# Performance work log

Measured on AMD Instinct MI355X. Metric: run time of the kernel, lower is better.

## Reference

```python
import jax, jax.numpy as jnp
import numpy as np

NUM_HEADS = 8
SIGMA = 1.0
LAMBDA_INIT = 0.1
GAMMA_INIT = 0.001


def _pos_encoding(H, W, d_model):
    # 2D sinusoidal encoding: first half encodes x (width), second half y (height)
    d = d_model // 2
    div = jnp.exp(jnp.arange(0, d, 2, dtype=jnp.float32) * (-np.log(10000.0) / d))
    xs = jnp.arange(W, dtype=jnp.float32)[:, None] * div  # (W, d//2)
    ys = jnp.arange(H, dtype=jnp.float32)[:, None] * div  # (H, d//2)
    pe_x = jnp.stack([jnp.sin(xs), jnp.cos(xs)], axis=-1).reshape(W, d)
    pe_y = jnp.stack([jnp.sin(ys), jnp.cos(ys)], axis=-1).reshape(H, d)
    pe = jnp.concatenate([
        jnp.broadcast_to(pe_x[None, :, :], (H, W, d)),
        jnp.broadcast_to(pe_y[:, None, :], (H, W, d)),
    ], axis=-1)
    return pe  # (H, W, d_model)


def _distance_map(H, W, sigma):
    # exp(-euclidean_dist / sigma) between all flattened pixel positions
    yy, xx = jnp.meshgrid(jnp.arange(H, dtype=jnp.float32), jnp.arange(W, dtype=jnp.float32), indexing='ij')
    coords = jnp.stack([yy.reshape(-1), xx.reshape(-1)], axis=-1)  # (HW, 2)
    d2 = jnp.sum((coords[:, None, :] - coords[None, :, :]) ** 2, axis=-1)
    return jnp.exp(-jnp.sqrt(d2) / sigma)  # (HW, HW)


def _conv1x1(x, w, b):
    # 1x1 conv == channel matmul; x: (B,C,H,W), w: (O,C), b: (O,)
    return jnp.einsum('bchw,oc->bohw', x, w) + b[None, :, None, None]


def setup_inputs() -> dict:
    key = jax.random.key(0)
    ks = jax.random.split(key, 9)
    B, C, H, W = 2, 256, 48, 48
    d_model = 256
    inp = {
        'x': jax.random.normal(ks[0], (B, C, H, W), dtype=jnp.float32),
        'Wq': jax.random.normal(ks[1], (d_model, C), dtype=jnp.float32) * 0.01,
        'bq': jnp.zeros((d_model,), dtype=jnp.float32),
        'Wk': jax.random.normal(ks[2], (d_model, C), dtype=jnp.float32) * 0.01,
        'bk': jnp.zeros((d_model,), dtype=jnp.float32),
        'Wv': jax.random.normal(ks[3], (d_model, C), dtype=jnp.float32) * 0.01,
        'bv': jnp.zeros((d_model,), dtype=jnp.float32),
        'Wo': jax.random.normal(ks[4], (C, d_model), dtype=jnp.float32) * 0.01,
        'bo': jnp.zeros((C,), dtype=jnp.float32),
        'lambda_dist': jnp.float32(LAMBDA_INIT),
        'gamma': jnp.float32(GAMMA_INIT),
    }
    return inp


def reference(x, Wq, bq, Wk, bk, Wv, bv, Wo, bo, lambda_dist, gamma):
    B, C, H, W = x.shape
    d_model = Wq.shape[0]
    d_k = d_model // NUM_HEADS
    pe = _pos_encoding(H, W, d_model).transpose(2, 0, 1)[None]  # (1, d_model, H, W)
    dm = _distance_map(H, W, SIGMA)                              # (HW, HW)

    q = _conv1x1(x, Wq, bq) + pe
    k = _conv1x1(x, Wk, bk) + pe
    v = _conv1x1(x, Wv, bv)

    def heads(t):
        return t.reshape(B, NUM_HEADS, d_k, H * W).transpose(0, 1, 3, 2)  # (B,h,HW,d_k)

    Q, K, V = heads(q), heads(k), heads(v)
    scores = jnp.einsum('bhnd,bhmd->bhnm', Q, K) / jnp.sqrt(jnp.float32(d_k))
    scores = scores + (lambda_dist * dm)[None, None]  # 'exp' distance prior bias
    attn = jax.nn.softmax(scores, axis=-1)
    out = jnp.einsum('bhnm,bhmd->bhnd', attn, V)
    out = out.transpose(0, 1, 3, 2).reshape(B, d_model, H, W)
    fused = gamma * out  # simple weighted fusion, single (self) branch
    return x + _conv1x1(fused, Wo, bo)
```

## Files before the change

### kernel.cpp

```cpp
#include <hip/hip_runtime.h>

#define HW 2304
#define SW 48
#define DMODEL 256
#define NHEADS 8
#define DK 32
#define BATCH 2

typedef unsigned short u16;
typedef __attribute__((ext_vector_type(8))) short short8;
typedef __attribute__((ext_vector_type(4))) float f32x4;

__device__ __forceinline__ float bf2f(u16 v) {
  union { unsigned int u; float f; } c; c.u = ((unsigned int)v) << 16; return c.f;
}
__device__ __forceinline__ float lo2f(unsigned int u) {
  union { unsigned int u; float f; } c; c.u = u << 16; return c.f;
}
__device__ __forceinline__ float hi2f(unsigned int u) {
  union { unsigned int u; float f; } c; c.u = u & 0xffff0000u; return c.f;
}
__device__ __forceinline__ u16 f2bf(float f) {
  union { unsigned int u; float f; } c; c.f = f;
  unsigned int u = c.u;
  unsigned int r = (u + 0x7FFFu + ((u >> 16) & 1u)) >> 16;
  return (u16)r;
}
__device__ __forceinline__ unsigned int pkbf(float a, float b) {
  union { float f; unsigned int u; } ca, cb;
  ca.f = a; cb.f = b;
  return __builtin_amdgcn_perm(ca.u, cb.u, 0x03020706u);
}
__device__ __forceinline__ float ex2(float x) {
#if __has_builtin(__builtin_amdgcn_exp2f)
  return __builtin_amdgcn_exp2f(x);
#else
  return __expf(x * 0.6931471805599453f);
#endif
}
__device__ __forceinline__ int div48(int n) { return (n * 87382) >> 22; }
__device__ __forceinline__ int div3(int n) { return (n * 171) >> 9; }
__device__ __forceinline__ int swz(int row, int k) {
  return ((row >> 4) << 12) + ((k >> 3) << 7) + ((row & 15) << 3) + (k & 7);
}

#define LOG2E 1.4426950408889634f

__global__ __launch_bounds__(256) void prep_kernel(
    const float* __restrict__ x,
    const float* __restrict__ Wq, const float* __restrict__ Wk,
    const float* __restrict__ Wv, const float* __restrict__ Wo,
    const float* __restrict__ lam_p,
    u16* __restrict__ xt, u16* __restrict__ Wb, u16* __restrict__ et) {
  int bid = blockIdx.x;
  int t = threadIdx.x;
  if (bid < 288) {
    int b = bid / 144, r = bid % 144;
    int c0 = (r / 36) * 64, n0 = (r % 36) * 64;
    __shared__ u16 sh[64][72];
#pragma unroll
    for (int p = 0; p < 4; ++p) {
      int row = (t >> 4) + p * 16;
      int col4 = (t & 15) * 4;
      float4 v = *(const float4*)(x + (size_t)(b * DMODEL + c0 + row) * HW +
                                  n0 + col4);
      sh[col4 + 0][row] = f2bf(v.x);
      sh[col4 + 1][row] = f2bf(v.y);
      sh[col4 + 2][row] = f2bf(v.z);
      sh[col4 + 3][row] = f2bf(v.w);
    }
    __syncthreads();
    u16* xtb = xt + (size_t)b * HW * DMODEL;
#pragma unroll
    for (int q = 0; q < 2; ++q) {
      int nrow = t >> 2;
      int c8 = (t & 3) * 8 + q * 32;
      *(uint4*)(xtb + swz(n0 + nrow, c0 + c8)) = *(const uint4*)&sh[nrow][c8];
    }
  } else if (bid < 544) {
    int idx = (bid - 288) * 1024 + t * 4;
    int which = idx >> 16, off = idx & 65535;
    int m = off >> 8, k = off & 255;
    const float* src = (which == 0) ? Wq : (which == 1) ? Wk
                       : (which == 2) ? Wv : Wo;
    float4 v = *(const float4*)(src + off);
    ushort4 ov;
    ov.x = f2bf(v.x); ov.y = f2bf(v.y); ov.z = f2bf(v.z); ov.w = f2bf(v.w);
    *(ushort4*)(Wb + which * 65536 + swz(m, k)) = ov;
  } else {
    int id = (bid - 544) * 256 + t;
    if (id < 15200) {
      int flat = id * 8;
      int tile = flat >> 8;
      int within = flat & 255;
      int a = within >> 4;
      int b0 = within & 15;
      int dyi = (tile * 205) >> 10;
      int dp = tile - dyi * 5;
      float dy = (float)(dyi - 47);
      float dy2 = dy * dy;
      int dxb = (dp - 2) * 16 + a - b0;
      float lam = lam_p[0] * LOG2E;
      u16 o[8];
#pragma unroll
      for (int j = 0; j < 8; ++j) {
        float dx = (float)(dxb - j);
        o[j] = f2bf(lam * __expf(-sqrtf(dy2 + dx * dx)));
      }
      *(uint4*)(et + flat) = *(const uint4*)o;
    }
  }
}

__global__ __launch_bounds__(256) void qkv_kernel(
    const u16* __restrict__ Wb, const u16* __restrict__ xt,
    const float* __restrict__ bq, const float* __restrict__ bk,
    const float* __restrict__ bv,
    u16* __restrict__ qt, u16* __restrict__ ktb, u16* __restrict__ vb) {
  int t = threadIdx.x;
  int w = t >> 6, lane = t & 63, lo = lane & 15, quad = lane >> 4;
  int n0 = blockIdx.x * 64;
  int mb = blockIdx.y, b = blockIdx.z;
  int which = mb >> 2;
  int mrel0 = (mb & 3) * 64;
  const u16* A = Wb + which * 65536 + ((mrel0 + w * 16) >> 4) * 4096 + lo * 8;
  const float* bias = (which == 0) ? bq : (which == 1) ? bk : bv;
  const u16* Bx = xt + (size_t)b * HW * DMODEL + lo * 8;

  f32x4 acc[4] = {{0.f, 0.f, 0.f, 0.f}, {0.f, 0.f, 0.f, 0.f},
                  {0.f, 0.f, 0.f, 0.f}, {0.f, 0.f, 0.f, 0.f}};
#pragma unroll
  for (int k0 = 0; k0 < DMODEL; k0 += 32) {
    int kblk = ((k0 >> 3) + quad) << 7;
    short8 af = *(const short8*)(A + kblk);
#pragma unroll
    for (int nt = 0; nt < 4; ++nt) {
      short8 bf_ = *(const short8*)(Bx + ((n0 + nt * 16) >> 4) * 4096 + kblk);
      acc[nt] = __builtin_amdgcn_mfma_f32_16x16x32_bf16(af, bf_, acc[nt], 0, 0, 0);
    }
  }

  int mbase = mrel0 + w * 16 + quad * 4;
  if (which == 2) {
#pragma unroll
    for (int reg = 0; reg < 4; ++reg) {
      int mrel = mbase + reg;
      float bi = bias[mrel];
      u16* dst = vb + (size_t)(b * DMODEL + mrel) * HW + n0 + lo;
#pragma unroll
      for (int nt = 0; nt < 4; ++nt) dst[nt * 16] = f2bf(acc[nt][reg] + bi);
    }
  } else {
    float sc = (which == 0) ? (0.17677669529663687f * LOG2E) : 1.0f;
    int h = mbase >> 5, d0 = mbase & 31;
    u16* base = ((which == 0) ? qt : ktb) + (size_t)(b * NHEADS + h) * HW * DK;
    float bi[4], dv[4];
    bool usecos[4], usey[4];
#pragma unroll
    for (int reg = 0; reg < 4; ++reg) {
      int mrel = mbase + reg;
      bi[reg] = bias[mrel];
      int oo = mrel & 127;
      dv[reg] = __expf(-0.07195578415606394f * (float)(oo & ~1));
      usecos[reg] = (oo & 1);
      usey[reg] = (mrel >= 128);
    }
#pragma unroll
    for (int nt = 0; nt < 4; ++nt) {
      int n = n0 + nt * 16 + lo;
      int yy = div48(n), xx = n - yy * SW;
      ushort4 ov;
      float vals[4];
#pragma unroll
      for (int reg = 0; reg < 4; ++reg) {
        float tv = (usey[reg] ? (float)yy : (float)xx) * dv[reg];
        float pe = usecos[reg] ? __cosf(tv) : __sinf(tv);
        vals[reg] = (acc[nt][reg] + bi[reg] + pe) * sc;
      }
      ov.x = f2bf(vals[0]); ov.y = f2bf(vals[1]);
      ov.z = f2bf(vals[2]); ov.w = f2bf(vals[3]);
      *(ushort4*)(base + (size_t)n * DK + d0) = ov;
    }
  }
}

__global__ __launch_bounds__(256) void attn_kernel(
    const u16* __restrict__ qt, const u16* __restrict__ ktb,
    const u16* __restrict__ vb, const u16* __restrict__ et,
    u16* __restrict__ po_o, float* __restrict__ po_l) {
  int t = threadIdx.x;
  int w = t >> 6;
  int lane = t & 63;
  int lo = lane & 15, quad = lane >> 4;
  int n0 = blockIdx.x * 64;
  int h = blockIdx.y >> 2, kh = blockIdx.y & 3;
  int b = blockIdx.z;

  __shared__ u16 Ks[2][64 * 40];
  __shared__ u16 Vs[2][32 * 72];

  const u16* qtg = qt + (size_t)(b * NHEADS + h) * HW * DK;
  const u16* ktg = ktb + (size_t)(b * NHEADS + h) * HW * DK;
  const u16* vbg = vb + (size_t)(b * DMODEL + h * DK) * HW;

  short8 qf = *(const short8*)(qtg + (size_t)(n0 + w * 16 + lo) * DK + quad * 8);

  int srow = t >> 2;
  int sks = srow >> 5, srr = srow & 31;
  int sv = (srr < 16) ? (8 * (srr >> 2) + (srr & 3))
                      : (8 * ((srr - 16) >> 2) + 4 + ((srr - 16) & 3));
  int skey = sks * 32 + sv;
  int sc8 = (t & 3) * 8;
  int vdd = t >> 3, vmo = (t & 7) * 8;

  int tq = (n0 >> 4) + w;
  int qh = quad >> 1;
  int yqt = div3(tq);
  int qcode = tq + 2 * yqt + 237;
  const u16* etb = et + lo * 16 + (quad & 1) * 8;

  union { unsigned int u[4]; short8 s; } onesu;
  onesu.u[0] = onesu.u[1] = onesu.u[2] = onesu.u[3] = 0x3F803F80u;
  const short8 onesf = onesu.s;

  f32x4 o0 = {0.f, 0.f, 0.f, 0.f}, o1 = {0.f, 0.f, 0.f, 0.f};
  f32x4 lacc = {0.f, 0.f, 0.f, 0.f};

  const int kt0 = kh * 9;
  {
    int m0 = kt0 * 64;
    *(uint4*)&Ks[0][srow * 40 + sc8] =
        *(const uint4*)(ktg + (size_t)(m0 + skey) * DK + sc8);
    *(uint4*)&Vs[0][vdd * 72 + vmo] =
        *(const uint4*)(vbg + (size_t)vdd * HW + m0 + vmo);
  }
  __syncthreads();

  for (int i = 0; i < 9; ++i) {
    int cur = i & 1;
    if (i + 1 < 9) {
      int m1 = (kt0 + i + 1) * 64;
      *(uint4*)&Ks[cur ^ 1][srow * 40 + sc8] =
          *(const uint4*)(ktg + (size_t)(m1 + skey) * DK + sc8);
      *(uint4*)&Vs[cur ^ 1][vdd * 72 + vmo] =
          *(const uint4*)(vbg + (size_t)vdd * HW + m1 + vmo);
    }

    int tm0 = (kt0 + i) * 4 + qh;
    int tm1 = tm0 + 2;
    int ym0 = div3(tm0), ym1 = div3(tm1);
    uint4 eb0 = *(const uint4*)(etb + (size_t)(qcode - tm0 - 2 * ym0) * 256);
    uint4 eb1 = *(const uint4*)(etb + (size_t)(qcode - tm1 - 2 * ym1) * 256);

#pragma unroll
    for (int ks = 0; ks < 2; ++ks) {
      uint4 ebv = ks ? eb1 : eb0;
      short8 kfA = *(const short8*)&Ks[cur][(ks * 32 + lo) * 40 + quad * 8];
      short8 kfB = *(const short8*)&Ks[cur][(ks * 32 + 16 + lo) * 40 + quad * 8];
      f32x4 zA = {lo2f(ebv.x), hi2f(ebv.x), lo2f(ebv.y), hi2f(ebv.y)};
      f32x4 zB = {lo2f(ebv.z), hi2f(ebv.z), lo2f(ebv.w), hi2f(ebv.w)};
      f32x4 sA = __builtin_amdgcn_mfma_f32_16x16x32_bf16(kfA, qf, zA, 0, 0, 0);
      f32x4 sB = __builtin_amdgcn_mfma_f32_16x16x32_bf16(kfB, qf, zB, 0, 0, 0);
      float p0 = ex2(sA[0]), p1 = ex2(sA[1]), p2 = ex2(sA[2]), p3 = ex2(sA[3]);
      float p4 = ex2(sB[0]), p5 = ex2(sB[1]), p6 = ex2(sB[2]), p7 = ex2(sB[3]);
      unsigned int pk32[4] = {pkbf(p0, p1), pkbf(p2, p3),
                              pkbf(p4, p5), pkbf(p6, p7)};
      short8 pfrag = *(const short8*)pk32;
      lacc = __builtin_amdgcn_mfma_f32_16x16x32_bf16(onesf, pfrag, lacc, 0, 0, 0);
      short8 v0 = *(const short8*)&Vs[cur][lo * 72 + ks * 32 + quad * 8];
      o0 = __builtin_amdgcn_mfma_f32_16x16x32_bf16(v0, pfrag, o0, 0, 0, 0);
      short8 v1 = *(const short8*)&Vs[cur][(16 + lo) * 72 + ks * 32 + quad * 8];
      o1 = __builtin_amdgcn_mfma_f32_16x16x32_bf16(v1, pfrag, o1, 0, 0, 0);
    }
    __syncthreads();
  }

  int slot = (b * NHEADS + h) * 36 + blockIdx.x;
  u16* pw = po_o + (size_t)(kh * 576 + slot) * 2048 + w * 512;
  uint2 s0, s1;
  s0.x = pkbf(o0[0], o0[1]); s0.y = pkbf(o0[2], o0[3]);
  s1.x = pkbf(o1[0], o1[1]); s1.y = pkbf(o1[2], o1[3]);
  *(uint2*)(pw + lane * 4) = s0;
  *(uint2*)(pw + 256 + lane * 4) = s1;
  if (quad == 0)
    po_l[(size_t)(kh * 576 + slot) * 64 + w * 16 + lo] = lacc[0];
}

__global__ __launch_bounds__(256) void out_kernel(
    const float* __restrict__ x, const u16* __restrict__ Wob,
    const float* __restrict__ bo, const float* __restrict__ gp,
    const u16* __restrict__ po_o, const float* __restrict__ po_l,
    float* __restrict__ out) {
  int t = threadIdx.x;
  int w = t >> 6, lane = t & 63, lo = lane & 15, quad = lane >> 4;
  int qt_ = blockIdx.x;
  int c0 = blockIdx.y * 64;
  int b = blockIdx.z;
  float gamma = gp[0];

  __shared__ u16 Bt[16384];

#pragma unroll 1
  for (int h = 0; h < NHEADS; ++h) {
    int slot = (b * NHEADS + h) * 36 + qt_;
    float s0[4] = {0.f, 0.f, 0.f, 0.f}, s1[4] = {0.f, 0.f, 0.f, 0.f};
    float lt = 0.f;
#pragma unroll
    for (int kh = 0; kh < 4; ++kh) {
      const u16* p = po_o + (size_t)(kh * 576 + slot) * 2048 + w * 512;
      ushort4 a0 = *(const ushort4*)(p + lane * 4);
      ushort4 a1 = *(const ushort4*)(p + 256 + lane * 4);
      s0[0] += bf2f(a0.x); s0[1] += bf2f(a0.y);
      s0[2] += bf2f(a0.z); s0[3] += bf2f(a0.w);
      s1[0] += bf2f(a1.x); s1[1] += bf2f(a1.y);
      s1[2] += bf2f(a1.z); s1[3] += bf2f(a1.w);
      lt += po_l[(size_t)(kh * 576 + slot) * 64 + w * 16 + lo];
    }
    float inv = 1.0f / lt;
    int base = w * 4096 + (h * 4 + (quad >> 1)) * 128 + lo * 8 + (quad & 1) * 4;
    ushort4 w0, w1;
    w0.x = f2bf(s0[0] * inv); w0.y = f2bf(s0[1] * inv);
    w0.z = f2bf(s0[2] * inv); w0.w = f2bf(s0[3] * inv);
    w1.x = f2bf(s1[0] * inv); w1.y = f2bf(s1[1] * inv);
    w1.z = f2bf(s1[2] * inv); w1.w = f2bf(s1[3] * inv);
    *(ushort4*)&Bt[base] = w0;
    *(ushort4*)&Bt[base + 256] = w1;
  }
  __syncthreads();

  const u16* A = Wob + ((c0 + w * 16) >> 4) * 4096 + lo * 8;
  f32x4 acc[4] = {{0.f, 0.f, 0.f, 0.f}, {0.f, 0.f, 0.f, 0.f},
                  {0.f, 0.f, 0.f, 0.f}, {0.f, 0.f, 0.f, 0.f}};
#pragma unroll
  for (int k0 = 0; k0 < DMODEL; k0 += 32) {
    int kblk = ((k0 >> 3) + quad) << 7;
    short8 af = *(const short8*)(A + kblk);
#pragma unroll
    for (int nt = 0; nt < 4; ++nt) {
      short8 bf_ = *(const short8*)&Bt[nt * 4096 + kblk + lo * 8];
      acc[nt] = __builtin_amdgcn_mfma_f32_16x16x32_bf16(af, bf_, acc[nt], 0, 0, 0);
    }
  }

  int n0 = qt_ * 64;
#pragma unroll
  for (int reg = 0; reg < 4; ++reg) {
    int c = c0 + w * 16 + quad * 4 + reg;
    float bi = bo[c];
    const float* xs = x + (size_t)(b * DMODEL + c) * HW + n0 + lo;
    float* os = out + (size_t)(b * DMODEL + c) * HW + n0 + lo;
#pragma unroll
    for (int nt = 0; nt < 4; ++nt)
      os[nt * 16] = xs[nt * 16] + gamma * acc[nt][reg] + bi;
  }
}

extern "C" void kernel_launch(void* const* d_in, const int* in_sizes, int n_in,
                              void* d_out, int out_size, void* d_ws,
                              size_t ws_size, hipStream_t stream) {
  const float* x   = (const float*)d_in[0];
  const float* Wq  = (const float*)d_in[1];
  const float* bq  = (const float*)d_in[2];
  const float* Wk  = (const float*)d_in[3];
  const float* bk  = (const float*)d_in[4];
  const float* Wv  = (const float*)d_in[5];
  const float* bv  = (const float*)d_in[6];
  const float* Wo  = (const float*)d_in[7];
  const float* bo  = (const float*)d_in[8];
  const float* lam = (const float*)d_in[9];
  const float* gam = (const float*)d_in[10];

  char* wsb = (char*)d_ws;
  u16* Wb  = (u16*)(wsb + 36864);
  u16* xt  = (u16*)(wsb + 561152);
  u16* qt  = (u16*)(wsb + 2920448);
  u16* ktb = (u16*)(wsb + 5279744);
  u16* vb  = (u16*)(wsb + 7639040);
  u16* et  = (u16*)(wsb + 9998336);
  u16* po_o = (u16*)(wsb + 20615168);
  float* po_l = (float*)(wsb + 30052352);
  float* out = (float*)d_out;

  prep_kernel<<<dim3(604), 256, 0, stream>>>(x, Wq, Wk, Wv, Wo, lam,
                                             xt, Wb, et);
  qkv_kernel<<<dim3(36, 12, BATCH), 256, 0, stream>>>(Wb, xt, bq, bk, bv,
                                                      qt, ktb, vb);
  attn_kernel<<<dim3(36, 32, BATCH), 256, 0, stream>>>(qt, ktb, vb, et,
                                                       po_o, po_l);
  out_kernel<<<dim3(36, 4, BATCH), 256, 0, stream>>>(x, Wb + 3 * 65536, bo, gam,
                                                     po_o, po_l, out);
}
```

Baseline: 124.7 us.

## Fuse bf16 conversion prep into QKV and out GEMMs; prefetch bias tiles in attention

Drops the separate prep kernel. The QKV kernel now converts its 64-column x tile to bf16 in shared memory and converts fp32 weight rows to bf16 on the fly, and also builds the distance-bias table in extra blocks. The out kernel likewise reads fp32 Wo directly. Inside attention, the next iteration's distance-bias values are loaded one step early, and the MFMA section runs at raised wave priority. This removes a kernel launch and the workspace round trip for xt and Wb, but x is re-read and re-converted by each of the 12 m-blocks with strided column loads, and weights are converted redundantly in every block.

```diff
diff --git a/kernel.cpp b/kernel.cpp
--- a/kernel.cpp
+++ b/kernel.cpp
@@ -43,52 +43,29 @@
 __device__ __forceinline__ int swz(int row, int k) {
   return ((row >> 4) << 12) + ((k >> 3) << 7) + ((row & 15) << 3) + (k & 7);
 }
+__device__ __forceinline__ short8 ldA8(const float* p) {
+  float4 a = *(const float4*)(p);
+  float4 c = *(const float4*)(p + 4);
+  u16 o[8];
+  o[0] = f2bf(a.x); o[1] = f2bf(a.y); o[2] = f2bf(a.z); o[3] = f2bf(a.w);
+  o[4] = f2bf(c.x); o[5] = f2bf(c.y); o[6] = f2bf(c.z); o[7] = f2bf(c.w);
+  return *(const short8*)o;
+}
 
 #define LOG2E 1.4426950408889634f
 
-__global__ __launch_bounds__(256) void prep_kernel(
+__global__ __launch_bounds__(256) void qkv_kernel(
     const float* __restrict__ x,
     const float* __restrict__ Wq, const float* __restrict__ Wk,
-    const float* __restrict__ Wv, const float* __restrict__ Wo,
-    const float* __restrict__ lam_p,
-    u16* __restrict__ xt, u16* __restrict__ Wb, u16* __restrict__ et) {
+    const float* __restrict__ Wv,
+    const float* __restrict__ bq, const float* __restrict__ bk,
+    const float* __restrict__ bv, const float* __restrict__ lam_p,
+    u16* __restrict__ qt, u16* __restrict__ ktb, u16* __restrict__ vb,
+    u16* __restrict__ et) {
   int bid = blockIdx.x;
   int t = threadIdx.x;
-  if (bid < 288) {
-    int b = bid / 144, r = bid % 144;
-    int c0 = (r / 36) * 64, n0 = (r % 36) * 64;
-    __shared__ u16 sh[64][72];
-#pragma unroll
-    for (int p = 0; p < 4; ++p) {
-      int row = (t >> 4) + p * 16;
-      int col4 = (t & 15) * 4;
-      float4 v = *(const float4*)(x + (size_t)(b * DMODEL + c0 + row) * HW +
-                                  n0 + col4);
-      sh[col4 + 0][row] = f2bf(v.x);
-      sh[col4 + 1][row] = f2bf(v.y);
-      sh[col4 + 2][row] = f2bf(v.z);
-      sh[col4 + 3][row] = f2bf(v.w);
-    }
-    __syncthreads();
-    u16* xtb = xt + (size_t)b * HW * DMODEL;
-#pragma unroll
-    for (int q = 0; q < 2; ++q) {
-      int nrow = t >> 2;
-      int c8 = (t & 3) * 8 + q * 32;
-      *(uint4*)(xtb + swz(n0 + nrow, c0 + c8)) = *(const uint4*)&sh[nrow][c8];
-    }
-  } else if (bid < 544) {
-    int idx = (bid - 288) * 1024 + t * 4;
-    int which = idx >> 16, off = idx & 65535;
-    int m = off >> 8, k = off & 255;
-    const float* src = (which == 0) ? Wq : (which == 1) ? Wk
-                       : (which == 2) ? Wv : Wo;
-    float4 v = *(const float4*)(src + off);
-    ushort4 ov;
-    ov.x = f2bf(v.x); ov.y = f2bf(v.y); ov.z = f2bf(v.z); ov.w = f2bf(v.w);
-    *(ushort4*)(Wb + which * 65536 + swz(m, k)) = ov;
-  } else {
-    int id = (bid - 544) * 256 + t;
+  if (bid >= 864) {
+    int id = (bid - 864) * 256 + t;
     if (id < 15200) {
       int flat = id * 8;
       int tile = flat >> 8;
@@ -109,33 +86,47 @@
       }
       *(uint4*)(et + flat) = *(const uint4*)o;
     }
-  }
-}
-
-__global__ __launch_bounds__(256) void qkv_kernel(
-    const u16* __restrict__ Wb, const u16* __restrict__ xt,
-    const float* __restrict__ bq, const float* __restrict__ bk,
-    const float* __restrict__ bv,
-    u16* __restrict__ qt, u16* __restrict__ ktb, u16* __restrict__ vb) {
-  int t = threadIdx.x;
+    return;
+  }
+
+  int tmp = bid / 36;
+  int nb = bid - tmp * 36;
+  int mb = tmp % 12;
+  int b = tmp / 12;
+  int n0 = nb * 64;
   int w = t >> 6, lane = t & 63, lo = lane & 15, quad = lane >> 4;
-  int n0 = blockIdx.x * 64;
-  int mb = blockIdx.y, b = blockIdx.z;
   int which = mb >> 2;
   int mrel0 = (mb & 3) * 64;
-  const u16* A = Wb + which * 65536 + ((mrel0 + w * 16) >> 4) * 4096 + lo * 8;
+
+  __shared__ u16 Bt[16384];
+
+  {
+    const float* xb = x + (size_t)b * DMODEL * HW + (size_t)(w * 64) * HW +
+                      n0 + lane;
+#pragma unroll
+    for (int j = 0; j < 8; ++j) {
+      u16 a8[8];
+#pragma unroll
+      for (int cc = 0; cc < 8; ++cc)
+        a8[cc] = f2bf(xb[(size_t)(j * 8 + cc) * HW]);
+      *(uint4*)&Bt[swz(lane, w * 64 + j * 8)] = *(const uint4*)a8;
+    }
+  }
+  __syncthreads();
+
+  const float* Wsrc = (which == 0) ? Wq : (which == 1) ? Wk : Wv;
   const float* bias = (which == 0) ? bq : (which == 1) ? bk : bv;
-  const u16* Bx = xt + (size_t)b * HW * DMODEL + lo * 8;
+  const float* Ar = Wsrc + (size_t)(mrel0 + w * 16 + lo) * DMODEL + quad * 8;
 
   f32x4 acc[4] = {{0.f, 0.f, 0.f, 0.f}, {0.f, 0.f, 0.f, 0.f},
                   {0.f, 0.f, 0.f, 0.f}, {0.f, 0.f, 0.f, 0.f}};
 #pragma unroll
   for (int k0 = 0; k0 < DMODEL; k0 += 32) {
+    short8 af = ldA8(Ar + k0);
     int kblk = ((k0 >> 3) + quad) << 7;
-    short8 af = *(const short8*)(A + kblk);
 #pragma unroll
     for (int nt = 0; nt < 4; ++nt) {
-      short8 bf_ = *(const short8*)(Bx + ((n0 + nt * 16) >> 4) * 4096 + kblk);
+      short8 bf_ = *(const short8*)&Bt[nt * 4096 + kblk + lo * 8];
       acc[nt] = __builtin_amdgcn_mfma_f32_16x16x32_bf16(af, bf_, acc[nt], 0, 0, 0);
     }
   }
@@ -227,6 +218,19 @@
   f32x4 lacc = {0.f, 0.f, 0.f, 0.f};
 
   const int kt0 = kh * 9;
+
+#define EBLOAD(d0_, d1_, tt_)                                            \
+  {                                                                      \
+    int tmA_ = (tt_);                                                    \
+    int tmB_ = tmA_ + 2;                                                 \
+    int ymA_ = div3(tmA_), ymB_ = div3(tmB_);                            \
+    d0_ = *(const uint4*)(etb + (size_t)(qcode - tmA_ - 2 * ymA_) * 256);\
+    d1_ = *(const uint4*)(etb + (size_t)(qcode - tmB_ - 2 * ymB_) * 256);\
+  }
+
+  uint4 ebA, ebB;
+  EBLOAD(ebA, ebB, kt0 * 4 + qh);
+  uint4 ebAn = ebA, ebBn = ebB;
   {
     int m0 = kt0 * 64;
     *(uint4*)&Ks[0][srow * 40 + sc8] =
@@ -244,17 +248,13 @@
           *(const uint4*)(ktg + (size_t)(m1 + skey) * DK + sc8);
       *(uint4*)&Vs[cur ^ 1][vdd * 72 + vmo] =
           *(const uint4*)(vbg + (size_t)vdd * HW + m1 + vmo);
-    }
-
-    int tm0 = (kt0 + i) * 4 + qh;
-    int tm1 = tm0 + 2;
-    int ym0 = div3(tm0), ym1 = div3(tm1);
-    uint4 eb0 = *(const uint4*)(etb + (size_t)(qcode - tm0 - 2 * ym0) * 256);
-    uint4 eb1 = *(const uint4*)(etb + (size_t)(qcode - tm1 - 2 * ym1) * 256);
-
+      EBLOAD(ebAn, ebBn, (kt0 + i + 1) * 4 + qh);
+    }
+
+    __builtin_amdgcn_s_setprio(1);
 #pragma unroll
     for (int ks = 0; ks < 2; ++ks) {
-      uint4 ebv = ks ? eb1 : eb0;
+      uint4 ebv = ks ? ebB : ebA;
       short8 kfA = *(const short8*)&Ks[cur][(ks * 32 + lo) * 40 + quad * 8];
       short8 kfB = *(const short8*)&Ks[cur][(ks * 32 + 16 + lo) * 40 + quad * 8];
       f32x4 zA = {lo2f(ebv.x), hi2f(ebv.x), lo2f(ebv.y), hi2f(ebv.y)};
@@ -272,8 +272,11 @@
       short8 v1 = *(const short8*)&Vs[cur][(16 + lo) * 72 + ks * 32 + quad * 8];
       o1 = __builtin_amdgcn_mfma_f32_16x16x32_bf16(v1, pfrag, o1, 0, 0, 0);
     }
+    __builtin_amdgcn_s_setprio(0);
     __syncthreads();
-  }
+    ebA = ebAn; ebB = ebBn;
+  }
+#undef EBLOAD
 
   int slot = (b * NHEADS + h) * 36 + blockIdx.x;
   u16* pw = po_o + (size_t)(kh * 576 + slot) * 2048 + w * 512;
@@ -287,7 +290,7 @@
 }
 
 __global__ __launch_bounds__(256) void out_kernel(
-    const float* __restrict__ x, const u16* __restrict__ Wob,
+    const float* __restrict__ x, const float* __restrict__ Wo,
     const float* __restrict__ bo, const float* __restrict__ gp,
     const u16* __restrict__ po_o, const float* __restrict__ po_l,
     float* __restrict__ out) {
@@ -328,13 +331,13 @@
   }
   __syncthreads();
 
-  const u16* A = Wob + ((c0 + w * 16) >> 4) * 4096 + lo * 8;
+  const float* Ar = Wo + (size_t)(c0 + w * 16 + lo) * DMODEL + quad * 8;
   f32x4 acc[4] = {{0.f, 0.f, 0.f, 0.f}, {0.f, 0.f, 0.f, 0.f},
                   {0.f, 0.f, 0.f, 0.f}, {0.f, 0.f, 0.f, 0.f}};
 #pragma unroll
   for (int k0 = 0; k0 < DMODEL; k0 += 32) {
+    short8 af = ldA8(Ar + k0);
     int kblk = ((k0 >> 3) + quad) << 7;
-    short8 af = *(const short8*)(A + kblk);
 #pragma unroll
     for (int nt = 0; nt < 4; ++nt) {
       short8 bf_ = *(const short8*)&Bt[nt * 4096 + kblk + lo * 8];
@@ -371,8 +374,6 @@
   const float* gam = (const float*)d_in[10];
 
   char* wsb = (char*)d_ws;
-  u16* Wb  = (u16*)(wsb + 36864);
-  u16* xt  = (u16*)(wsb + 561152);
   u16* qt  = (u16*)(wsb + 2920448);
   u16* ktb = (u16*)(wsb + 5279744);
   u16* vb  = (u16*)(wsb + 7639040);
@@ -381,12 +382,10 @@
   float* po_l = (float*)(wsb + 30052352);
   float* out = (float*)d_out;
 
-  prep_kernel<<<dim3(604), 256, 0, stream>>>(x, Wq, Wk, Wv, Wo, lam,
-                                             xt, Wb, et);
-  qkv_kernel<<<dim3(36, 12, BATCH), 256, 0, stream>>>(Wb, xt, bq, bk, bv,
-                                                      qt, ktb, vb);
+  qkv_kernel<<<dim3(924), 256, 0, stream>>>(x, Wq, Wk, Wv, bq, bk, bv, lam,
+                                            qt, ktb, vb, et);
   attn_kernel<<<dim3(36, 32, BATCH), 256, 0, stream>>>(qt, ktb, vb, et,
                                                        po_o, po_l);
-  out_kernel<<<dim3(36, 4, BATCH), 256, 0, stream>>>(x, Wb + 3 * 65536, bo, gam,
+  out_kernel<<<dim3(36, 4, BATCH), 256, 0, stream>>>(x, Wo, bo, gam,
                                                      po_o, po_l, out);
 }
```

Measured after the change: 126.1 us. No clear change (+1.1%).

## Drop split-K in attention; normalize in-kernel and write swizzled output directly

Applied to the files above, without the earlier changes.

The attention kernel no longer splits the key range into four partitions. Each block now walks all 36 key tiles, normalizes by the row sum itself and writes the bf16 result in a swizzled layout. The output kernel then reads MFMA operands straight from global memory, with no partial-sum reduction or shared-memory staging. This removes the partial-result traffic and the reduction, but the attention grid shrinks from 2304 to 576 blocks, so there is less parallelism to hide latency on a GPU with many CUs.

```diff
diff --git a/kernel.cpp b/kernel.cpp
--- a/kernel.cpp
+++ b/kernel.cpp
@@ -187,13 +187,13 @@
 __global__ __launch_bounds__(256) void attn_kernel(
     const u16* __restrict__ qt, const u16* __restrict__ ktb,
     const u16* __restrict__ vb, const u16* __restrict__ et,
-    u16* __restrict__ po_o, float* __restrict__ po_l) {
+    u16* __restrict__ aot) {
   int t = threadIdx.x;
   int w = t >> 6;
   int lane = t & 63;
   int lo = lane & 15, quad = lane >> 4;
   int n0 = blockIdx.x * 64;
-  int h = blockIdx.y >> 2, kh = blockIdx.y & 3;
+  int h = blockIdx.y;
   int b = blockIdx.z;
 
   __shared__ u16 Ks[2][64 * 40];
@@ -226,27 +226,25 @@
   f32x4 o0 = {0.f, 0.f, 0.f, 0.f}, o1 = {0.f, 0.f, 0.f, 0.f};
   f32x4 lacc = {0.f, 0.f, 0.f, 0.f};
 
-  const int kt0 = kh * 9;
   {
-    int m0 = kt0 * 64;
     *(uint4*)&Ks[0][srow * 40 + sc8] =
-        *(const uint4*)(ktg + (size_t)(m0 + skey) * DK + sc8);
+        *(const uint4*)(ktg + (size_t)skey * DK + sc8);
     *(uint4*)&Vs[0][vdd * 72 + vmo] =
-        *(const uint4*)(vbg + (size_t)vdd * HW + m0 + vmo);
+        *(const uint4*)(vbg + (size_t)vdd * HW + vmo);
   }
   __syncthreads();
 
-  for (int i = 0; i < 9; ++i) {
+  for (int i = 0; i < 36; ++i) {
     int cur = i & 1;
-    if (i + 1 < 9) {
-      int m1 = (kt0 + i + 1) * 64;
+    if (i + 1 < 36) {
+      int m1 = (i + 1) * 64;
       *(uint4*)&Ks[cur ^ 1][srow * 40 + sc8] =
           *(const uint4*)(ktg + (size_t)(m1 + skey) * DK + sc8);
       *(uint4*)&Vs[cur ^ 1][vdd * 72 + vmo] =
           *(const uint4*)(vbg + (size_t)vdd * HW + m1 + vmo);
     }
 
-    int tm0 = (kt0 + i) * 4 + qh;
+    int tm0 = i * 4 + qh;
     int tm1 = tm0 + 2;
     int ym0 = div3(tm0), ym1 = div3(tm1);
     uint4 eb0 = *(const uint4*)(etb + (size_t)(qcode - tm0 - 2 * ym0) * 256);
@@ -275,60 +273,31 @@
     __syncthreads();
   }
 
-  int slot = (b * NHEADS + h) * 36 + blockIdx.x;
-  u16* pw = po_o + (size_t)(kh * 576 + slot) * 2048 + w * 512;
-  uint2 s0, s1;
-  s0.x = pkbf(o0[0], o0[1]); s0.y = pkbf(o0[2], o0[3]);
-  s1.x = pkbf(o1[0], o1[1]); s1.y = pkbf(o1[2], o1[3]);
-  *(uint2*)(pw + lane * 4) = s0;
-  *(uint2*)(pw + 256 + lane * 4) = s1;
-  if (quad == 0)
-    po_l[(size_t)(kh * 576 + slot) * 64 + w * 16 + lo] = lacc[0];
+  float inv = 1.0f / lacc[0];
+  int n = n0 + w * 16 + lo;
+  u16* aog = aot + (size_t)b * HW * DMODEL;
+  ushort4 w0, w1;
+  w0.x = f2bf(o0[0] * inv); w0.y = f2bf(o0[1] * inv);
+  w0.z = f2bf(o0[2] * inv); w0.w = f2bf(o0[3] * inv);
+  w1.x = f2bf(o1[0] * inv); w1.y = f2bf(o1[1] * inv);
+  w1.z = f2bf(o1[2] * inv); w1.w = f2bf(o1[3] * inv);
+  *(ushort4*)&aog[swz(n, h * DK + quad * 4)] = w0;
+  *(ushort4*)&aog[swz(n, h * DK + 16 + quad * 4)] = w1;
 }
 
 __global__ __launch_bounds__(256) void out_kernel(
     const float* __restrict__ x, const u16* __restrict__ Wob,
     const float* __restrict__ bo, const float* __restrict__ gp,
-    const u16* __restrict__ po_o, const float* __restrict__ po_l,
-    float* __restrict__ out) {
+    const u16* __restrict__ aot, float* __restrict__ out) {
   int t = threadIdx.x;
   int w = t >> 6, lane = t & 63, lo = lane & 15, quad = lane >> 4;
-  int qt_ = blockIdx.x;
+  int n0 = blockIdx.x * 64;
   int c0 = blockIdx.y * 64;
   int b = blockIdx.z;
   float gamma = gp[0];
-
-  __shared__ u16 Bt[16384];
-
-#pragma unroll 1
-  for (int h = 0; h < NHEADS; ++h) {
-    int slot = (b * NHEADS + h) * 36 + qt_;
-    float s0[4] = {0.f, 0.f, 0.f, 0.f}, s1[4] = {0.f, 0.f, 0.f, 0.f};
-    float lt = 0.f;
-#pragma unroll
-    for (int kh = 0; kh < 4; ++kh) {
-      const u16* p = po_o + (size_t)(kh * 576 + slot) * 2048 + w * 512;
-      ushort4 a0 = *(const ushort4*)(p + lane * 4);
-      ushort4 a1 = *(const ushort4*)(p + 256 + lane * 4);
-      s0[0] += bf2f(a0.x); s0[1] += bf2f(a0.y);
-      s0[2] += bf2f(a0.z); s0[3] += bf2f(a0.w);
-      s1[0] += bf2f(a1.x); s1[1] += bf2f(a1.y);
-      s1[2] += bf2f(a1.z); s1[3] += bf2f(a1.w);
-      lt += po_l[(size_t)(kh * 576 + slot) * 64 + w * 16 + lo];
-    }
-    float inv = 1.0f / lt;
-    int base = w * 4096 + (h * 4 + (quad >> 1)) * 128 + lo * 8 + (quad & 1) * 4;
-    ushort4 w0, w1;
-    w0.x = f2bf(s0[0] * inv); w0.y = f2bf(s0[1] * inv);
-    w0.z = f2bf(s0[2] * inv); w0.w = f2bf(s0[3] * inv);
-    w1.x = f2bf(s1[0] * inv); w1.y = f2bf(s1[1] * inv);
-    w1.z = f2bf(s1[2] * inv); w1.w = f2bf(s1[3] * inv);
-    *(ushort4*)&Bt[base] = w0;
-    *(ushort4*)&Bt[base + 256] = w1;
-  }
-  __syncthreads();
-
   const u16* A = Wob + ((c0 + w * 16) >> 4) * 4096 + lo * 8;
+  const u16* Ba = aot + (size_t)b * HW * DMODEL + lo * 8;
+
   f32x4 acc[4] = {{0.f, 0.f, 0.f, 0.f}, {0.f, 0.f, 0.f, 0.f},
                   {0.f, 0.f, 0.f, 0.f}, {0.f, 0.f, 0.f, 0.f}};
 #pragma unroll
@@ -337,12 +306,11 @@
     short8 af = *(const short8*)(A + kblk);
 #pragma unroll
     for (int nt = 0; nt < 4; ++nt) {
-      short8 bf_ = *(const short8*)&Bt[nt * 4096 + kblk + lo * 8];
+      short8 bf_ = *(const short8*)(Ba + ((n0 + nt * 16) >> 4) * 4096 + kblk);
       acc[nt] = __builtin_amdgcn_mfma_f32_16x16x32_bf16(af, bf_, acc[nt], 0, 0, 0);
     }
   }
 
-  int n0 = qt_ * 64;
 #pragma unroll
   for (int reg = 0; reg < 4; ++reg) {
     int c = c0 + w * 16 + quad * 4 + reg;
@@ -377,16 +345,15 @@
   u16* ktb = (u16*)(wsb + 5279744);
   u16* vb  = (u16*)(wsb + 7639040);
   u16* et  = (u16*)(wsb + 9998336);
-  u16* po_o = (u16*)(wsb + 20615168);
-  float* po_l = (float*)(wsb + 30052352);
+  u16* aot = (u16*)(wsb + 20615168);
   float* out = (float*)d_out;
 
   prep_kernel<<<dim3(604), 256, 0, stream>>>(x, Wq, Wk, Wv, Wo, lam,
                                              xt, Wb, et);
   qkv_kernel<<<dim3(36, 12, BATCH), 256, 0, stream>>>(Wb, xt, bq, bk, bv,
                                                       qt, ktb, vb);
-  attn_kernel<<<dim3(36, 32, BATCH), 256, 0, stream>>>(qt, ktb, vb, et,
-                                                       po_o, po_l);
+  attn_kernel<<<dim3(36, NHEADS, BATCH), 256, 0, stream>>>(qt, ktb, vb, et,
+                                                           aot);
   out_kernel<<<dim3(36, 4, BATCH), 256, 0, stream>>>(x, Wb + 3 * 65536, bo, gam,
-                                                     po_o, po_l, out);
-}
+                                                     aot, out);
+}
```

New measurement: 137.1 us. +9.9%, slower.
